# Optimization experiments

Hardware: AMD Instinct MI355X
Metric: run time of the kernel (lower is better)

Reference implementation:

```python
import jax, jax.numpy as jnp
import numpy as np

N, E, G, L = 100000, 1600000, 2000, 2000
IN, H1, H2, H3, OUT = 128, 64, 32, 16, 16
EPS = 1e-5


def _layernorm(x, g, b):
    m = jnp.mean(x, axis=-1, keepdims=True)
    v = jnp.mean(jnp.square(x - m), axis=-1, keepdims=True)
    return (x - m) * jax.lax.rsqrt(v + EPS) * g + b


def _gcn_block(x, W, b, Wr, br, g, beta, src, dst, deg_inv_sqrt):
    # GCNConv with added self-loops and symmetric normalization (PyG default)
    h = x @ W  # [N, F]
    coef = (deg_inv_sqrt[src] * deg_inv_sqrt[dst])[:, None]  # [E, 1]
    msg = h[src] * coef  # [E, F] -- dominant memory traffic
    agg = jax.ops.segment_sum(msg, dst, num_segments=N)
    agg = agg + h * jnp.square(deg_inv_sqrt)[:, None] + b  # self-loop term + bias
    out = agg + (x @ Wr + br)  # residual projection
    return jax.nn.relu(_layernorm(out, g, beta))


def setup_inputs():
    key = jax.random.key(0)
    ks = jax.random.split(key, 40)
    w = lambda k, i, o: jax.random.normal(k, (i, o), jnp.float32) / np.sqrt(i)
    d = {}
    d['x'] = jax.random.normal(ks[0], (N, IN), jnp.float32)
    d['src'] = jax.random.randint(ks[1], (E,), 0, N, jnp.int32)
    d['dst'] = jax.random.randint(ks[2], (E,), 0, N, jnp.int32)
    d['batch'] = jnp.sort(jax.random.randint(ks[3], (N,), 0, G, jnp.int32))
    d['link_idx'] = jax.random.randint(ks[4], (2, L), 0, G, jnp.int32)
    dims = [(IN, H1), (H1, H2), (H2, H3), (H3, OUT)]
    for i, (fi, fo) in enumerate(dims, 1):
        d[f'W{i}'] = w(ks[5 + 4 * i], fi, fo)
        d[f'b{i}'] = jnp.zeros((fo,), jnp.float32)
        d[f'Wr{i}'] = w(ks[6 + 4 * i], fi, fo)
        d[f'br{i}'] = jnp.zeros((fo,), jnp.float32)
        d[f'g{i}'] = jnp.ones((fo,), jnp.float32)
        d[f'bt{i}'] = jnp.zeros((fo,), jnp.float32)
    d['Wm1'] = w(ks[30], 2 * OUT, OUT)
    d['bm1'] = jnp.zeros((OUT,), jnp.float32)
    d['Wm2'] = w(ks[31], OUT, OUT // 2)
    d['bm2'] = jnp.zeros((OUT // 2,), jnp.float32)
    d['Wm3'] = w(ks[32], OUT // 2, 1)
    d['bm3'] = jnp.zeros((1,), jnp.float32)
    return d


def reference(x, src, dst, batch, link_idx,
              W1, b1, Wr1, br1, g1, bt1,
              W2, b2, Wr2, br2, g2, bt2,
              W3, b3, Wr3, br3, g3, bt3,
              W4, b4, Wr4, br4, g4, bt4,
              Wm1, bm1, Wm2, bm2, Wm3, bm3):
    ones_e = jnp.ones((E,), jnp.float32)
    deg = jax.ops.segment_sum(ones_e, dst, num_segments=N) + 1.0  # + self-loop
    dis = jax.lax.rsqrt(deg)
    h = _gcn_block(x, W1, b1, Wr1, br1, g1, bt1, src, dst, dis)
    h = _gcn_block(h, W2, b2, Wr2, br2, g2, bt2, src, dst, dis)
    h = _gcn_block(h, W3, b3, Wr3, br3, g3, bt3, src, dst, dis)
    h = _gcn_block(h, W4, b4, Wr4, br4, g4, bt4, src, dst, dis)
    # global mean pool over subgraphs
    cnt = jax.ops.segment_sum(jnp.ones((N,), jnp.float32), batch, num_segments=G)
    gemb = jax.ops.segment_sum(h, batch, num_segments=G) / jnp.maximum(cnt, 1.0)[:, None]
    feat = jnp.concatenate([gemb[link_idx[0]], gemb[link_idx[1]]], axis=1)  # [L, 2*OUT]
    z = jax.nn.relu(feat @ Wm1 + bm1)
    z = jax.nn.relu(z @ Wm2 + bm2)
    z = z @ Wm3 + bm3
    return jax.nn.sigmoid(z).squeeze(-1)  # [L]
```

## Files before the change

### kernel.cpp

```cpp
#include <hip/hip_runtime.h>
#include <math.h>

namespace {

constexpr int N = 100000;
constexpr int E = 1600000;
constexpr int G = 2000;
constexpr int L = 2000;

constexpr int SCAN_CHUNK = 1024;
constexpr int NB = (N + SCAN_CHUNK - 1) / SCAN_CHUNK;


__global__ void hist_kernel(const int* __restrict__ dst, int* __restrict__ deg) {
  int i = blockIdx.x * blockDim.x + threadIdx.x;
  if (i < E) atomicAdd(&deg[dst[i]], 1);
}

__global__ void scan1_kernel(const int* __restrict__ deg, int* __restrict__ bsum) {
  const int t = threadIdx.x;
  const int base = blockIdx.x * SCAN_CHUNK + t * 4;
  int s = 0;
  if (base < N) {
    const int4 v = *reinterpret_cast<const int4*>(deg + base);
    s = v.x + v.y + v.z + v.w;
  }
  __shared__ int ss[256];
  ss[t] = s;
  __syncthreads();
#pragma unroll
  for (int off = 128; off >= 1; off >>= 1) {
    if (t < off) ss[t] += ss[t + off];
    __syncthreads();
  }
  if (t == 0) bsum[blockIdx.x] = ss[0];
}

__global__ void scan2_kernel(const int* __restrict__ bsum, int* __restrict__ boff) {
  __shared__ int ss[128];
  const int t = threadIdx.x;
  ss[t] = (t < NB) ? bsum[t] : 0;
  __syncthreads();
#pragma unroll
  for (int off = 1; off < 128; off <<= 1) {
    int v = (t >= off) ? ss[t - off] : 0;
    __syncthreads();
    ss[t] += v;
    __syncthreads();
  }
  if (t < NB) boff[t] = (t == 0) ? 0 : ss[t - 1];
}

__global__ void scan3_kernel(const int* __restrict__ deg, const int* __restrict__ boff,
                             int* __restrict__ row_ptr, int* __restrict__ cursor,
                             float* __restrict__ dis) {
  const int t = threadIdx.x;
  const int base = blockIdx.x * SCAN_CHUNK + t * 4;
  int d0 = 0, d1 = 0, d2 = 0, d3 = 0;
  if (base < N) {
    const int4 v = *reinterpret_cast<const int4*>(deg + base);
    d0 = v.x; d1 = v.y; d2 = v.z; d3 = v.w;
  }
  const int tsum = d0 + d1 + d2 + d3;
  __shared__ int ss[256];
  ss[t] = tsum;
  __syncthreads();
#pragma unroll
  for (int off = 1; off < 256; off <<= 1) {
    int v = (t >= off) ? ss[t - off] : 0;
    __syncthreads();
    ss[t] += v;
    __syncthreads();
  }
  if (base < N) {
    const int p0 = ((t == 0) ? 0 : ss[t - 1]) + boff[blockIdx.x];
    const int p1 = p0 + d0;
    const int p2 = p1 + d1;
    const int p3 = p2 + d2;
    *reinterpret_cast<int4*>(row_ptr + base) = make_int4(p0, p1, p2, p3);
    *reinterpret_cast<int4*>(cursor + base) = make_int4(p0, p1, p2, p3);
    const float4 dv = make_float4(rsqrtf((float)d0 + 1.0f), rsqrtf((float)d1 + 1.0f),
                                  rsqrtf((float)d2 + 1.0f), rsqrtf((float)d3 + 1.0f));
    *reinterpret_cast<float4*>(dis + base) = dv;
  }
  if (blockIdx.x == 0 && t == 0) row_ptr[N] = E;
}

__global__ void fill_kernel(const int* __restrict__ src, const int* __restrict__ dst,
                            const float* __restrict__ dis, int* __restrict__ cursor,
                            int* __restrict__ col, float* __restrict__ cf) {
  int e = blockIdx.x * blockDim.x + threadIdx.x;
  if (e < E) {
    const int s = src[e];
    const int d = dst[e];
    const int pos = atomicAdd(&cursor[d], 1);
    col[pos] = s;
    cf[pos] = dis[s] * dis[d];
  }
}


__device__ __forceinline__ void f4fma(float4& a, float s, const float4 w) {
  a.x = fmaf(s, w.x, a.x);
  a.y = fmaf(s, w.y, a.y);
  a.z = fmaf(s, w.z, a.z);
  a.w = fmaf(s, w.w, a.w);
}

template <int FI, int FO>
__global__ __launch_bounds__(1024) void gemm2_kernel(const float* __restrict__ x,
                                                     const float* __restrict__ W,
                                                     const float* __restrict__ Wr,
                                                     float* __restrict__ h,
                                                     float* __restrict__ r) {
  __shared__ float sW[FI * FO];
  __shared__ float sWr[FI * FO];
  for (int i = threadIdx.x; i < FI * FO; i += blockDim.x) {
    sW[i] = W[i];
    sWr[i] = Wr[i];
  }
  __syncthreads();
  constexpr int CG = FO / 4;
  const int total = (N / 4) * CG;
  const int stride = gridDim.x * blockDim.x;
  for (int idx = blockIdx.x * blockDim.x + threadIdx.x; idx < total; idx += stride) {
    const int rb = idx / CG;
    const int col = (idx - rb * CG) * 4;
    const int row0 = rb * 4;
    float4 aH[4], aR[4];
#pragma unroll
    for (int i = 0; i < 4; ++i) {
      aH[i] = make_float4(0.f, 0.f, 0.f, 0.f);
      aR[i] = make_float4(0.f, 0.f, 0.f, 0.f);
    }
    const float* xr = x + (size_t)row0 * FI;
#pragma unroll
    for (int k = 0; k < FI; k += 4) {
      float xs[4][4];
#pragma unroll
      for (int i = 0; i < 4; ++i) {
        const float4 xv = *reinterpret_cast<const float4*>(xr + i * FI + k);
        xs[i][0] = xv.x; xs[i][1] = xv.y; xs[i][2] = xv.z; xs[i][3] = xv.w;
      }
#pragma unroll
      for (int kk = 0; kk < 4; ++kk) {
        const float4 w4 = *reinterpret_cast<const float4*>(&sW[(k + kk) * FO + col]);
        const float4 w4r = *reinterpret_cast<const float4*>(&sWr[(k + kk) * FO + col]);
#pragma unroll
        for (int i = 0; i < 4; ++i) {
          f4fma(aH[i], xs[i][kk], w4);
          f4fma(aR[i], xs[i][kk], w4r);
        }
      }
    }
#pragma unroll
    for (int i = 0; i < 4; ++i) {
      *reinterpret_cast<float4*>(&h[(size_t)(row0 + i) * FO + col]) = aH[i];
      *reinterpret_cast<float4*>(&r[(size_t)(row0 + i) * FO + col]) = aR[i];
    }
  }
}


template <int FO, bool POOL>
__global__ void gcn_agg_kernel(const int* __restrict__ row_ptr, const int* __restrict__ col,
                               const float* __restrict__ cf, const float* __restrict__ h,
                               const float* __restrict__ r, const float* __restrict__ dis,
                               const float* __restrict__ b, const float* __restrict__ br,
                               const float* __restrict__ g, const float* __restrict__ bt,
                               float* __restrict__ out, const int* __restrict__ batch,
                               float* __restrict__ gemb, float* __restrict__ cnt) {
  constexpr int NPW = 64 / FO;
  const int lane = threadIdx.x & 63;
  const int f = lane & (FO - 1);
  const int sub = lane / FO;
  const int waveId = (blockIdx.x * blockDim.x + threadIdx.x) >> 6;
  const int nWaves = (gridDim.x * blockDim.x) >> 6;
  const int nGroups = N / NPW;
  const float bf = b[f], brf = br[f], gf = g[f], btf = bt[f];
  for (int w = waveId; w < nGroups; w += nWaves) {
    const int node = w * NPW + sub;
    const int beg = row_ptr[node];
    const int end = row_ptr[node + 1];
    float acc = 0.f, acc2 = 0.f;
    int k = beg;
    for (; k + 1 < end; k += 2) {
      const int s0 = col[k];
      const int s1 = col[k + 1];
      const float c0 = cf[k];
      const float c1 = cf[k + 1];
      acc = fmaf(h[(size_t)s0 * FO + f], c0, acc);
      acc2 = fmaf(h[(size_t)s1 * FO + f], c1, acc2);
    }
    if (k < end) acc = fmaf(h[(size_t)col[k] * FO + f], cf[k], acc);
    acc += acc2;
    const float dv = dis[node];
    const size_t base = (size_t)node * FO + f;
    const float v = acc + h[base] * (dv * dv) + bf + r[base] + brf;
    float s = v;
#pragma unroll
    for (int m = FO / 2; m >= 1; m >>= 1) s += __shfl_xor(s, m, 64);
    const float mean = s * (1.0f / FO);
    const float d0 = v - mean;
    float vs = d0 * d0;
#pragma unroll
    for (int m = FO / 2; m >= 1; m >>= 1) vs += __shfl_xor(vs, m, 64);
    const float var = vs * (1.0f / FO);
    float o = d0 * rsqrtf(var + 1e-5f) * gf + btf;
    o = fmaxf(o, 0.f);
    if (POOL) {
      const int bb = batch[node];
      atomicAdd(&gemb[bb * FO + f], o);
      if (f == 0) atomicAdd(&cnt[bb], 1.0f);
    } else {
      out[base] = o;
    }
  }
}


__global__ void gdiv_kernel(float* __restrict__ gemb, const float* __restrict__ cnt) {
  const int idx = blockIdx.x * blockDim.x + threadIdx.x;
  if (idx < G * 16) gemb[idx] /= fmaxf(cnt[idx >> 4], 1.0f);
}

__global__ void mlp_kernel(const float* __restrict__ gemb, const int* __restrict__ link,
                           const float* __restrict__ Wm1, const float* __restrict__ bm1,
                           const float* __restrict__ Wm2, const float* __restrict__ bm2,
                           const float* __restrict__ Wm3, const float* __restrict__ bm3,
                           float* __restrict__ out) {
  __shared__ float sW1[32 * 16], sW2[16 * 8], sW3[8], sb1[16], sb2[8], sb3;
  for (int i = threadIdx.x; i < 32 * 16; i += blockDim.x) sW1[i] = Wm1[i];
  for (int i = threadIdx.x; i < 16 * 8; i += blockDim.x) sW2[i] = Wm2[i];
  if (threadIdx.x < 8) {
    sW3[threadIdx.x] = Wm3[threadIdx.x];
    sb2[threadIdx.x] = bm2[threadIdx.x];
  }
  if (threadIdx.x < 16) sb1[threadIdx.x] = bm1[threadIdx.x];
  if (threadIdx.x == 0) sb3 = bm3[0];
  __syncthreads();
  const int l = blockIdx.x * blockDim.x + threadIdx.x;
  if (l >= L) return;
  const int a = link[l];
  const int c = link[L + l];
  float feat[32];
#pragma unroll
  for (int k = 0; k < 16; ++k) feat[k] = gemb[a * 16 + k];
#pragma unroll
  for (int k = 0; k < 16; ++k) feat[16 + k] = gemb[c * 16 + k];
  float z1[16];
#pragma unroll
  for (int j = 0; j < 16; ++j) {
    float s = sb1[j];
#pragma unroll
    for (int k = 0; k < 32; ++k) s = fmaf(feat[k], sW1[k * 16 + j], s);
    z1[j] = fmaxf(s, 0.f);
  }
  float z2[8];
#pragma unroll
  for (int j = 0; j < 8; ++j) {
    float s = sb2[j];
#pragma unroll
    for (int k = 0; k < 16; ++k) s = fmaf(z1[k], sW2[k * 8 + j], s);
    z2[j] = fmaxf(s, 0.f);
  }
  float z3 = sb3;
#pragma unroll
  for (int k = 0; k < 8; ++k) z3 = fmaf(z2[k], sW3[k], z3);
  out[l] = 1.f / (1.f + expf(-z3));
}

}

extern "C" void kernel_launch(void* const* d_in, const int* in_sizes, int n_in,
                              void* d_out, int out_size, void* d_ws, size_t ws_size,
                              hipStream_t stream) {
  (void)in_sizes; (void)n_in; (void)out_size; (void)ws_size;
  const float* x = (const float*)d_in[0];
  const int* src = (const int*)d_in[1];
  const int* dst = (const int*)d_in[2];
  const int* batch = (const int*)d_in[3];
  const int* link = (const int*)d_in[4];
  const float *Wl[4], *bl[4], *Wrl[4], *brl[4], *gl[4], *btl[4];
  for (int i = 0; i < 4; ++i) {
    Wl[i] = (const float*)d_in[5 + 6 * i + 0];
    bl[i] = (const float*)d_in[5 + 6 * i + 1];
    Wrl[i] = (const float*)d_in[5 + 6 * i + 2];
    brl[i] = (const float*)d_in[5 + 6 * i + 3];
    gl[i] = (const float*)d_in[5 + 6 * i + 4];
    btl[i] = (const float*)d_in[5 + 6 * i + 5];
  }
  const float* Wm1 = (const float*)d_in[29];
  const float* bm1 = (const float*)d_in[30];
  const float* Wm2 = (const float*)d_in[31];
  const float* bm2 = (const float*)d_in[32];
  const float* Wm3 = (const float*)d_in[33];
  const float* bm3 = (const float*)d_in[34];
  float* out = (float*)d_out;

  char* wsb = (char*)d_ws;
  int* deg_i = (int*)wsb;
  int* row_ptr = deg_i + N;
  int* cursor = row_ptr + (N + 1);
  float* dis = (float*)(cursor + N);
  int* bsum = (int*)(dis + N);
  int* boff = bsum + NB;
  int* col = boff + NB;
  float* cf = (float*)(col + E);
  float* bufA = cf + E;
  float* bufB = bufA + (size_t)N * 64;
  float* bufC = bufB + (size_t)N * 64;
  float* gemb = bufC + (size_t)N * 64;
  float* cnt = gemb + (size_t)G * 16;

  hipMemsetAsync(deg_i, 0, N * sizeof(int), stream);
  hist_kernel<<<(E + 255) / 256, 256, 0, stream>>>(dst, deg_i);
  scan1_kernel<<<NB, 256, 0, stream>>>(deg_i, bsum);
  scan2_kernel<<<1, 128, 0, stream>>>(bsum, boff);
  scan3_kernel<<<NB, 256, 0, stream>>>(deg_i, boff, row_ptr, cursor, dis);
  fill_kernel<<<(E + 255) / 256, 256, 0, stream>>>(src, dst, dis, cursor, col, cf);

  const int AGG_BLOCKS = 2048;

  gemm2_kernel<128, 64><<<((N / 4) * 16 + 1023) / 1024, 1024, 0, stream>>>(x, Wl[0], Wrl[0], bufA, bufB);
  gcn_agg_kernel<64, false><<<AGG_BLOCKS, 256, 0, stream>>>(row_ptr, col, cf, bufA, bufB, dis,
                                                            bl[0], brl[0], gl[0], btl[0], bufC,
                                                            batch, gemb, cnt);
  gemm2_kernel<64, 32><<<((N / 4) * 8 + 1023) / 1024, 1024, 0, stream>>>(bufC, Wl[1], Wrl[1], bufA, bufB);
  gcn_agg_kernel<32, false><<<AGG_BLOCKS, 256, 0, stream>>>(row_ptr, col, cf, bufA, bufB, dis,
                                                            bl[1], brl[1], gl[1], btl[1], bufC,
                                                            batch, gemb, cnt);
  gemm2_kernel<32, 16><<<((N / 4) * 4 + 1023) / 1024, 1024, 0, stream>>>(bufC, Wl[2], Wrl[2], bufA, bufB);
  gcn_agg_kernel<16, false><<<AGG_BLOCKS, 256, 0, stream>>>(row_ptr, col, cf, bufA, bufB, dis,
                                                            bl[2], brl[2], gl[2], btl[2], bufC,
                                                            batch, gemb, cnt);
  hipMemsetAsync(gemb, 0, (size_t)(G * 16 + G) * sizeof(float), stream);
  gemm2_kernel<16, 16><<<((N / 4) * 4 + 1023) / 1024, 1024, 0, stream>>>(bufC, Wl[3], Wrl[3], bufA, bufB);
  gcn_agg_kernel<16, true><<<AGG_BLOCKS, 256, 0, stream>>>(row_ptr, col, cf, bufA, bufB, dis,
                                                           bl[3], brl[3], gl[3], btl[3], nullptr,
                                                           batch, gemb, cnt);
  gdiv_kernel<<<(G * 16 + 255) / 256, 256, 0, stream>>>(gemb, cnt);
  mlp_kernel<<<(L + 255) / 256, 256, 0, stream>>>(gemb, link, Wm1, bm1, Wm2, bm2, Wm3, bm3, out);
}
```

Before: 735.0 us.

## Fold symmetric GCN normalization into GEMM output, drop per-edge coefficient array

```diff
diff --git a/kernel.cpp b/kernel.cpp
--- a/kernel.cpp
+++ b/kernel.cpp
@@ -87,15 +87,13 @@
 }
 
 __global__ void fill_kernel(const int* __restrict__ src, const int* __restrict__ dst,
-                            const float* __restrict__ dis, int* __restrict__ cursor,
-                            int* __restrict__ col, float* __restrict__ cf) {
+                            int* __restrict__ cursor, int* __restrict__ col) {
   int e = blockIdx.x * blockDim.x + threadIdx.x;
   if (e < E) {
     const int s = src[e];
     const int d = dst[e];
     const int pos = atomicAdd(&cursor[d], 1);
     col[pos] = s;
-    cf[pos] = dis[s] * dis[d];
   }
 }
 
@@ -111,7 +109,8 @@
 __global__ __launch_bounds__(1024) void gemm2_kernel(const float* __restrict__ x,
                                                      const float* __restrict__ W,
                                                      const float* __restrict__ Wr,
-                                                     float* __restrict__ h,
+                                                     const float* __restrict__ dis,
+                                                     float* __restrict__ hd,
                                                      float* __restrict__ r) {
   __shared__ float sW[FI * FO];
   __shared__ float sWr[FI * FO];
@@ -153,9 +152,13 @@
         }
       }
     }
+    const float4 dv = *reinterpret_cast<const float4*>(dis + row0);
+    const float dl[4] = {dv.x, dv.y, dv.z, dv.w};
 #pragma unroll
     for (int i = 0; i < 4; ++i) {
-      *reinterpret_cast<float4*>(&h[(size_t)(row0 + i) * FO + col]) = aH[i];
+      float4 o = aH[i];
+      o.x *= dl[i]; o.y *= dl[i]; o.z *= dl[i]; o.w *= dl[i];
+      *reinterpret_cast<float4*>(&hd[(size_t)(row0 + i) * FO + col]) = o;
       *reinterpret_cast<float4*>(&r[(size_t)(row0 + i) * FO + col]) = aR[i];
     }
   }
@@ -164,8 +167,8 @@
 
 template <int FO, bool POOL>
 __global__ void gcn_agg_kernel(const int* __restrict__ row_ptr, const int* __restrict__ col,
-                               const float* __restrict__ cf, const float* __restrict__ h,
-                               const float* __restrict__ r, const float* __restrict__ dis,
+                               const float* __restrict__ hd, const float* __restrict__ r,
+                               const float* __restrict__ dis,
                                const float* __restrict__ b, const float* __restrict__ br,
                                const float* __restrict__ g, const float* __restrict__ bt,
                                float* __restrict__ out, const int* __restrict__ batch,
@@ -187,16 +190,14 @@
     for (; k + 1 < end; k += 2) {
       const int s0 = col[k];
       const int s1 = col[k + 1];
-      const float c0 = cf[k];
-      const float c1 = cf[k + 1];
-      acc = fmaf(h[(size_t)s0 * FO + f], c0, acc);
-      acc2 = fmaf(h[(size_t)s1 * FO + f], c1, acc2);
-    }
-    if (k < end) acc = fmaf(h[(size_t)col[k] * FO + f], cf[k], acc);
+      acc += hd[(size_t)s0 * FO + f];
+      acc2 += hd[(size_t)s1 * FO + f];
+    }
+    if (k < end) acc += hd[(size_t)col[k] * FO + f];
     acc += acc2;
     const float dv = dis[node];
     const size_t base = (size_t)node * FO + f;
-    const float v = acc + h[base] * (dv * dv) + bf + r[base] + brf;
+    const float v = fmaf(dv, acc + hd[base], bf + r[base] + brf);
     float s = v;
 #pragma unroll
     for (int m = FO / 2; m >= 1; m >>= 1) s += __shfl_xor(s, m, 64);
@@ -306,8 +307,7 @@
   int* bsum = (int*)(dis + N);
   int* boff = bsum + NB;
   int* col = boff + NB;
-  float* cf = (float*)(col + E);
-  float* bufA = cf + E;
+  float* bufA = (float*)(col + E);
   float* bufB = bufA + (size_t)N * 64;
   float* bufC = bufB + (size_t)N * 64;
   float* gemb = bufC + (size_t)N * 64;
@@ -318,25 +318,25 @@
   scan1_kernel<<<NB, 256, 0, stream>>>(deg_i, bsum);
   scan2_kernel<<<1, 128, 0, stream>>>(bsum, boff);
   scan3_kernel<<<NB, 256, 0, stream>>>(deg_i, boff, row_ptr, cursor, dis);
-  fill_kernel<<<(E + 255) / 256, 256, 0, stream>>>(src, dst, dis, cursor, col, cf);
+  fill_kernel<<<(E + 255) / 256, 256, 0, stream>>>(src, dst, cursor, col);
 
   const int AGG_BLOCKS = 2048;
 
-  gemm2_kernel<128, 64><<<((N / 4) * 16 + 1023) / 1024, 1024, 0, stream>>>(x, Wl[0], Wrl[0], bufA, bufB);
-  gcn_agg_kernel<64, false><<<AGG_BLOCKS, 256, 0, stream>>>(row_ptr, col, cf, bufA, bufB, dis,
+  gemm2_kernel<128, 64><<<((N / 4) * 16 + 1023) / 1024, 1024, 0, stream>>>(x, Wl[0], Wrl[0], dis, bufA, bufB);
+  gcn_agg_kernel<64, false><<<AGG_BLOCKS, 256, 0, stream>>>(row_ptr, col, bufA, bufB, dis,
                                                             bl[0], brl[0], gl[0], btl[0], bufC,
                                                             batch, gemb, cnt);
-  gemm2_kernel<64, 32><<<((N / 4) * 8 + 1023) / 1024, 1024, 0, stream>>>(bufC, Wl[1], Wrl[1], bufA, bufB);
-  gcn_agg_kernel<32, false><<<AGG_BLOCKS, 256, 0, stream>>>(row_ptr, col, cf, bufA, bufB, dis,
+  gemm2_kernel<64, 32><<<((N / 4) * 8 + 1023) / 1024, 1024, 0, stream>>>(bufC, Wl[1], Wrl[1], dis, bufA, bufB);
+  gcn_agg_kernel<32, false><<<AGG_BLOCKS, 256, 0, stream>>>(row_ptr, col, bufA, bufB, dis,
                                                             bl[1], brl[1], gl[1], btl[1], bufC,
                                                             batch, gemb, cnt);
-  gemm2_kernel<32, 16><<<((N / 4) * 4 + 1023) / 1024, 1024, 0, stream>>>(bufC, Wl[2], Wrl[2], bufA, bufB);
-  gcn_agg_kernel<16, false><<<AGG_BLOCKS, 256, 0, stream>>>(row_ptr, col, cf, bufA, bufB, dis,
+  gemm2_kernel<32, 16><<<((N / 4) * 4 + 1023) / 1024, 1024, 0, stream>>>(bufC, Wl[2], Wrl[2], dis, bufA, bufB);
+  gcn_agg_kernel<16, false><<<AGG_BLOCKS, 256, 0, stream>>>(row_ptr, col, bufA, bufB, dis,
                                                             bl[2], brl[2], gl[2], btl[2], bufC,
                                                             batch, gemb, cnt);
   hipMemsetAsync(gemb, 0, (size_t)(G * 16 + G) * sizeof(float), stream);
-  gemm2_kernel<16, 16><<<((N / 4) * 4 + 1023) / 1024, 1024, 0, stream>>>(bufC, Wl[3], Wrl[3], bufA, bufB);
-  gcn_agg_kernel<16, true><<<AGG_BLOCKS, 256, 0, stream>>>(row_ptr, col, cf, bufA, bufB, dis,
+  gemm2_kernel<16, 16><<<((N / 4) * 4 + 1023) / 1024, 1024, 0, stream>>>(bufC, Wl[3], Wrl[3], dis, bufA, bufB);
+  gcn_agg_kernel<16, true><<<AGG_BLOCKS, 256, 0, stream>>>(row_ptr, col, bufA, bufB, dis,
                                                            bl[3], brl[3], gl[3], btl[3], nullptr,
                                                            batch, gemb, cnt);
   gdiv_kernel<<<(G * 16 + 255) / 256, 256, 0, stream>>>(gemb, cnt);
```

Result: slower. 790.8 us (+7.6%).
